# Performance work log

Hardware: AMD Instinct MI355X
Metric: run time of the kernel (lower is better)

## Reference

```python
import jax, jax.numpy as jnp
import numpy as np

B, N, C = 4, 2048, 128
H = 4
HD = C // H
SCALE = HD ** -0.5
NEG = -9e15


def setup_inputs() -> dict:
    key = jax.random.key(0)
    ks = jax.random.split(key, 6)
    x = jax.random.normal(ks[0], (B, N, C), dtype=jnp.float32)
    A = jax.random.randint(ks[1], (N, N), 0, 2, dtype=jnp.int32)
    std = 0.02
    Wq = jax.random.normal(ks[2], (C, C), dtype=jnp.float32) * std
    Wkv = jax.random.normal(ks[3], (2 * C, C), dtype=jnp.float32) * std
    Wp = jax.random.normal(ks[4], (C, C), dtype=jnp.float32) * std
    bp = jnp.zeros((C,), dtype=jnp.float32)
    return {"x": x, "A": A, "Wq": Wq, "Wkv": Wkv, "Wp": Wp, "bp": bp}


def reference(x, A, Wq, Wkv, Wp, bp):
    # q/k/v projections (torch Linear: x @ W.T)
    q = (x @ Wq.T).reshape(B, N, H, HD).transpose(0, 2, 1, 3)      # [B,H,N,HD]
    kv = (x @ Wkv.T).reshape(B, N, 2, H, HD).transpose(2, 0, 3, 1, 4)
    k, v = kv[0], kv[1]                                            # [B,H,N,HD]
    attn = jnp.einsum('bhnd,bhmd->bhnm', q, k) * SCALE             # [B,H,N,N]
    attn = jnp.where(A > 0, attn, NEG)                             # adjacency mask
    attn = jax.nn.softmax(attn, axis=-1)
    out = jnp.einsum('bhnm,bhmd->bhnd', attn, v)                   # [B,H,N,HD]
    out = out.transpose(0, 2, 1, 3).reshape(B, N, C)
    out = out @ Wp.T + bp
    return out + x                                                 # residual
```

## Files before the change

### kernel.cpp

```cpp
#include <hip/hip_runtime.h>
#include <math.h>

constexpr int kB = 4, kN = 2048, kC = 128, kH = 4, kHD = 32;
constexpr float kScaleLog2e = 0.17677669529663687f * 1.4426950408889634f;

typedef __attribute__((ext_vector_type(8))) short bf16x8;
typedef __attribute__((ext_vector_type(4))) float f32x4;

__device__ __forceinline__ float exp2fast(float x) { return __builtin_amdgcn_exp2f(x); }
__device__ __forceinline__ unsigned int cvtpk(float lo, float hi) {
  unsigned int r;
  asm("v_cvt_pk_bf16_f32 %0, %1, %2" : "=v"(r) : "v"(lo), "v"(hi));
  return r;
}
__device__ __forceinline__ float bflo(unsigned int u) {
  union { unsigned int u; float f; } v; v.u = u << 16; return v.f;
}
__device__ __forceinline__ float bfhi(unsigned int u) {
  union { unsigned int u; float f; } v; v.u = u & 0xFFFF0000u; return v.f;
}

__global__ __launch_bounds__(256) void qkv_abit_kernel(
    const float* __restrict__ x, const float* __restrict__ Wq,
    const float* __restrict__ Wkv, const int* __restrict__ A,
    unsigned short* __restrict__ qws, unsigned short* __restrict__ kws,
    unsigned short* __restrict__ vtws, unsigned long long* __restrict__ Abits) {
  const int bid = blockIdx.x;
  const int t = threadIdx.x;
  if (bid >= 512) {
    const int lane = t & 63;
    const int w0 = (bid - 512) * 4 + (t >> 6);
    for (int idx = w0; idx < kN * 32; idx += 2048) {
      const int row = idx >> 5, c0 = (idx & 31) * 64;
      unsigned long long msk = __ballot(A[(size_t)row * kN + c0 + lane] > 0);
      if (lane == 0) Abits[idx] = msk;
    }
    return;
  }
  __shared__ unsigned short xs[16][136];
  const int row0 = bid * 16;
  const int b = row0 >> 11;
  {
    const int r = t >> 4, c = (t & 15) * 8;
    const float* src = x + (size_t)(row0 + r) * kC + c;
    float4 a = *(const float4*)src;
    float4 bb = *(const float4*)(src + 4);
    *(uint4*)&xs[r][c] = make_uint4(cvtpk(a.x, a.y), cvtpk(a.z, a.w),
                                    cvtpk(bb.x, bb.y), cvtpk(bb.z, bb.w));
  }
  __syncthreads();
  const int w = t >> 6, l = t & 63, lr = l & 15, g = l >> 4;
  bf16x8 xf[4];
  #pragma unroll
  for (int s = 0; s < 4; ++s) xf[s] = *(const bf16x8*)&xs[lr][s * 32 + g * 8];
  #pragma unroll
  for (int ci = 0; ci < 6; ++ci) {
    const int c0 = (w * 6 + ci) * 16;
    const float* wrow = (c0 < 128) ? (Wq + (size_t)(c0 + lr) * kC)
                                   : (Wkv + (size_t)(c0 - 128 + lr) * kC);
    f32x4 acc = {0.f, 0.f, 0.f, 0.f};
    if (c0 < 256) {
      #pragma unroll
      for (int s = 0; s < 4; ++s) {
        const float* wp = wrow + s * 32 + g * 8;
        float4 wa = *(const float4*)wp, wb = *(const float4*)(wp + 4);
        union { uint4 u; bf16x8 v; } cw;
        cw.u = make_uint4(cvtpk(wa.x, wa.y), cvtpk(wa.z, wa.w),
                          cvtpk(wb.x, wb.y), cvtpk(wb.z, wb.w));
        acc = __builtin_amdgcn_mfma_f32_16x16x32_bf16(cw.v, xf[s], acc, 0, 0, 0);
      }
      if (c0 < 128) {
        #pragma unroll
        for (int i = 0; i < 4; ++i) acc[i] *= kScaleLog2e;
      }
      const int col0 = c0 + g * 4;
      const int h = (col0 & 127) >> 5, hd0 = col0 & 31;
      unsigned short* dst = (col0 < 128) ? qws : kws;
      uint2 pk = make_uint2(cvtpk(acc[0], acc[1]), cvtpk(acc[2], acc[3]));
      *(uint2*)&dst[((size_t)(b * kH + h) * kN + row0 + lr) * kHD + hd0] = pk;
    } else {
      #pragma unroll
      for (int s = 0; s < 4; ++s) {
        const float* wp = wrow + s * 32 + g * 8;
        float4 wa = *(const float4*)wp, wb = *(const float4*)(wp + 4);
        union { uint4 u; bf16x8 v; } cw;
        cw.u = make_uint4(cvtpk(wa.x, wa.y), cvtpk(wa.z, wa.w),
                          cvtpk(wb.x, wb.y), cvtpk(wb.z, wb.w));
        acc = __builtin_amdgcn_mfma_f32_16x16x32_bf16(xf[s], cw.v, acc, 0, 0, 0);
      }
      const int d = (c0 - 256) + lr;
      uint2 pk = make_uint2(cvtpk(acc[0], acc[1]), cvtpk(acc[2], acc[3]));
      *(uint2*)&vtws[((size_t)(b * kH + (d >> 5)) * kHD + (d & 31)) * kN + row0 + g * 4] = pk;
    }
  }
}

__global__ __launch_bounds__(256) void attn_kernel(
    const unsigned short* __restrict__ qws, const unsigned short* __restrict__ kws,
    const unsigned short* __restrict__ vtws,
    const unsigned long long* __restrict__ Abits,
    unsigned short* __restrict__ Opart, float* __restrict__ lws, int tiles) {
  __shared__ unsigned short Ksf[2][4][64][8];
  __shared__ unsigned short Vtf[2][2][2][64][8];
  __shared__ unsigned short Psf[4][2][64][8];
  const int t = threadIdx.x, w = t >> 6, l = t & 63, lr = l & 15, g = l >> 4;
  const int bh = blockIdx.y, q0 = blockIdx.x * 64, z = blockIdx.z;
  const int q = q0 + w * 16 + lr;
  const int kt0 = z * tiles;
  const unsigned short* kbase = kws + (size_t)bh * kN * kHD;
  const unsigned short* vbase = vtws + (size_t)bh * kHD * kN;
  bf16x8 qf = *(const bf16x8*)&qws[((size_t)bh * kN + q) * kHD + g * 8];
  const unsigned long long* arow = Abits + (size_t)q * (kN / 64);

  const int skc = t >> 6, sl = t & 63;
  const size_t koff = ((size_t)(skc * 16 + (sl & 15))) * kHD + (sl >> 4) * 8;
  const int sdh = t >> 7, sct = (t >> 6) & 1;
  const size_t voff = ((size_t)(sdh * 16 + (sl & 15))) * kN + sct * 32 + (sl >> 4) * 8;

  bf16x8 kreg = *(const bf16x8*)(kbase + (size_t)kt0 * 64 * kHD + koff);
  bf16x8 vreg = *(const bf16x8*)(vbase + (size_t)kt0 * 64 + voff);
  *(bf16x8*)&Ksf[0][skc][sl][0] = kreg;
  *(bf16x8*)&Vtf[0][sdh][sct][sl][0] = vreg;
  unsigned long long mw = arow[kt0], mwn = 0;

  f32x4 o0 = {0.f, 0.f, 0.f, 0.f}, o1 = {0.f, 0.f, 0.f, 0.f}, o2 = {0.f, 0.f, 0.f, 0.f};
  bf16x8 ones;
  #pragma unroll
  for (int i = 0; i < 8; ++i) ones[i] = (short)0x3F80;
  const int gsh = g * 4;
  unsigned short* const psw = &Psf[w][0][0][0];
  const int pbase = (((g >> 1) << 4) | lr) * 8 + (g & 1) * 4;

  for (int it = 0; it < tiles; ++it) {
    const int c = it & 1;
    const int kt = kt0 + it;
    __syncthreads();
    if (it + 1 < tiles) {
      kreg = *(const bf16x8*)(kbase + (size_t)(kt + 1) * 64 * kHD + koff);
      vreg = *(const bf16x8*)(vbase + (size_t)(kt + 1) * 64 + voff);
      mwn = arow[kt + 1];
    }
    const unsigned int wlo = ((unsigned int)mw) >> gsh;
    const unsigned int whi = ((unsigned int)(mw >> 32)) >> gsh;

    #pragma unroll
    for (int kc = 0; kc < 4; ++kc) {
      bf16x8 kf = *(const bf16x8*)&Ksf[c][kc][l][0];
      f32x4 acc = {0.f, 0.f, 0.f, 0.f};
      acc = __builtin_amdgcn_mfma_f32_16x16x32_bf16(kf, qf, acc, 0, 0, 0);
      const unsigned int word = (kc < 2) ? wlo : whi;
      float p[4];
      #pragma unroll
      for (int i = 0; i < 4; ++i) {
        float e = exp2fast(acc[i]);
        int msk;
        asm("v_bfe_i32 %0, %1, %2, 1" : "=v"(msk) : "v"(word), "n"((kc & 1) * 16 + i));
        union { float f; int u; } pu; pu.f = e;
        pu.u &= msk;
        p[i] = pu.f;
      }
      uint2 pk = make_uint2(cvtpk(p[0], p[1]), cvtpk(p[2], p[3]));
      *(uint2*)(psw + kc * 256 + pbase) = pk;
    }
    #pragma unroll
    for (int ct = 0; ct < 2; ++ct) {
      bf16x8 pf = *(const bf16x8*)&Psf[w][ct][l][0];
      bf16x8 va = *(const bf16x8*)&Vtf[c][0][ct][l][0];
      bf16x8 vb = *(const bf16x8*)&Vtf[c][1][ct][l][0];
      o0 = __builtin_amdgcn_mfma_f32_16x16x32_bf16(va, pf, o0, 0, 0, 0);
      o1 = __builtin_amdgcn_mfma_f32_16x16x32_bf16(vb, pf, o1, 0, 0, 0);
      o2 = __builtin_amdgcn_mfma_f32_16x16x32_bf16(ones, pf, o2, 0, 0, 0);
    }
    if (it + 1 < tiles) {
      *(bf16x8*)&Ksf[c ^ 1][skc][sl][0] = kreg;
      *(bf16x8*)&Vtf[c ^ 1][sdh][sct][sl][0] = vreg;
      mw = mwn;
    }
  }

  unsigned short* orow = Opart + ((size_t)(z * 16 + bh) * kN + q) * kHD;
  uint2 wa = make_uint2(cvtpk(o0[0], o0[1]), cvtpk(o0[2], o0[3]));
  uint2 wb = make_uint2(cvtpk(o1[0], o1[1]), cvtpk(o1[2], o1[3]));
  *(uint2*)&orow[g * 4] = wa;
  *(uint2*)&orow[16 + g * 4] = wb;
  if (g == 0) lws[(size_t)(z * 16 + bh) * kN + q] = o2[0];
}

__global__ __launch_bounds__(256) void proj_kernel(
    const unsigned short* __restrict__ Opart, const float* __restrict__ lws,
    const float* __restrict__ Wp, const float* __restrict__ bp,
    const float* __restrict__ x, float* __restrict__ out, int np) {
  const int t = threadIdx.x, w = t >> 6, l = t & 63, lr = l & 15, g = l >> 4;
  const int row0 = blockIdx.x * 16;
  const int b = row0 >> 11;
  bf16x8 af[4];
  #pragma unroll
  for (int s = 0; s < 4; ++s) {
    const int bh = b * kH + s;
    float a0 = 0.f, a1 = 0.f, a2 = 0.f, a3 = 0.f, a4 = 0.f, a5 = 0.f, a6 = 0.f, a7 = 0.f;
    float lacc = 0.f;
    for (int p = 0; p < np; ++p) {
      const size_t base = (size_t)(p * 16 + bh) * kN + row0 + lr;
      const uint4 u = *(const uint4*)&Opart[base * kHD + g * 8];
      lacc += lws[base];
      a0 += bflo(u.x); a1 += bfhi(u.x);
      a2 += bflo(u.y); a3 += bfhi(u.y);
      a4 += bflo(u.z); a5 += bfhi(u.z);
      a6 += bflo(u.w); a7 += bfhi(u.w);
    }
    const float inv = 1.f / fmaxf(lacc, 1e-30f);
    union { uint4 u; bf16x8 v; } cv;
    cv.u = make_uint4(cvtpk(a0 * inv, a1 * inv), cvtpk(a2 * inv, a3 * inv),
                      cvtpk(a4 * inv, a5 * inv), cvtpk(a6 * inv, a7 * inv));
    af[s] = cv.v;
  }
  #pragma unroll
  for (int ci = 0; ci < 2; ++ci) {
    const int c0 = (w * 2 + ci) * 16;
    const float* wrow = Wp + (size_t)(c0 + lr) * kC;
    f32x4 acc = {0.f, 0.f, 0.f, 0.f};
    #pragma unroll
    for (int s = 0; s < 4; ++s) {
      const float* wp = wrow + s * 32 + g * 8;
      float4 wa = *(const float4*)wp, wb = *(const float4*)(wp + 4);
      union { uint4 u; bf16x8 v; } cw;
      cw.u = make_uint4(cvtpk(wa.x, wa.y), cvtpk(wa.z, wa.w),
                        cvtpk(wb.x, wb.y), cvtpk(wb.z, wb.w));
      acc = __builtin_amdgcn_mfma_f32_16x16x32_bf16(cw.v, af[s], acc, 0, 0, 0);
    }
    const int col0 = c0 + g * 4;
    const size_t off = (size_t)(row0 + lr) * kC + col0;
    const float4 xb = *(const float4*)&x[off];
    const float4 bb = *(const float4*)&bp[col0];
    float4 r;
    r.x = acc[0] + bb.x + xb.x;
    r.y = acc[1] + bb.y + xb.y;
    r.z = acc[2] + bb.z + xb.z;
    r.w = acc[3] + bb.w + xb.w;
    *(float4*)&out[off] = r;
  }
}

extern "C" void kernel_launch(void* const* d_in, const int* in_sizes, int n_in,
                              void* d_out, int out_size, void* d_ws, size_t ws_size,
                              hipStream_t stream) {
  const float* x   = (const float*)d_in[0];
  const int*   A   = (const int*)d_in[1];
  const float* Wq  = (const float*)d_in[2];
  const float* Wkv = (const float*)d_in[3];
  const float* Wp  = (const float*)d_in[4];
  const float* bp  = (const float*)d_in[5];
  float* out = (float*)d_out;
  char* ws = (char*)d_ws;

  unsigned short* qws   = (unsigned short*)(ws);
  unsigned short* kws   = (unsigned short*)(ws + (2u << 20));
  unsigned short* vtws  = (unsigned short*)(ws + (4u << 20));
  unsigned long long* Abits = (unsigned long long*)(ws + (6u << 20));
  float*          lws   = (float*)(ws + (7u << 20));
  unsigned short* Opart = (unsigned short*)(ws + (8u << 20));

  const int np = (ws_size >= (16u << 20)) ? 4 : 1;
  const int tiles = 32 / np;

  qkv_abit_kernel<<<dim3(1024), dim3(256), 0, stream>>>(
      x, Wq, Wkv, A, qws, kws, vtws, Abits);
  attn_kernel<<<dim3(32, 16, np), dim3(256), 0, stream>>>(
      qws, kws, vtws, Abits, Opart, lws, tiles);
  proj_kernel<<<dim3(512), dim3(256), 0, stream>>>(Opart, lws, Wp, bp, x, out, np);
}
```

Before: 66.27 us.

## Process two query sub-tiles per wave to double K/V reuse in attention

Each wave in the attention kernel now handles 32 query rows (two 16-row MFMA tiles) instead of 16, sharing the K and V tiles loaded into LDS. The block covers 128 queries and the grid's x-dimension is halved. This amortizes K/V global loads, LDS staging and barriers over twice the work. In exchange it raises register and LDS use per block and halves the number of blocks, which may reduce occupancy or latency hiding.

```diff
diff --git a/kernel.cpp b/kernel.cpp
--- a/kernel.cpp
+++ b/kernel.cpp
@@ -102,15 +102,17 @@
     unsigned short* __restrict__ Opart, float* __restrict__ lws, int tiles) {
   __shared__ unsigned short Ksf[2][4][64][8];
   __shared__ unsigned short Vtf[2][2][2][64][8];
-  __shared__ unsigned short Psf[4][2][64][8];
+  __shared__ unsigned short Psf[4][2][2][64][8];
   const int t = threadIdx.x, w = t >> 6, l = t & 63, lr = l & 15, g = l >> 4;
-  const int bh = blockIdx.y, q0 = blockIdx.x * 64, z = blockIdx.z;
-  const int q = q0 + w * 16 + lr;
+  const int bh = blockIdx.y, q0 = blockIdx.x * 128, z = blockIdx.z;
+  const int qa = q0 + w * 32 + lr, qb = qa + 16;
   const int kt0 = z * tiles;
   const unsigned short* kbase = kws + (size_t)bh * kN * kHD;
   const unsigned short* vbase = vtws + (size_t)bh * kHD * kN;
-  bf16x8 qf = *(const bf16x8*)&qws[((size_t)bh * kN + q) * kHD + g * 8];
-  const unsigned long long* arow = Abits + (size_t)q * (kN / 64);
+  bf16x8 qf0 = *(const bf16x8*)&qws[((size_t)bh * kN + qa) * kHD + g * 8];
+  bf16x8 qf1 = *(const bf16x8*)&qws[((size_t)bh * kN + qb) * kHD + g * 8];
+  const unsigned long long* arow0 = Abits + (size_t)qa * (kN / 64);
+  const unsigned long long* arow1 = Abits + (size_t)qb * (kN / 64);
 
   const int skc = t >> 6, sl = t & 63;
   const size_t koff = ((size_t)(skc * 16 + (sl & 15))) * kHD + (sl >> 4) * 8;
@@ -121,14 +123,16 @@
   bf16x8 vreg = *(const bf16x8*)(vbase + (size_t)kt0 * 64 + voff);
   *(bf16x8*)&Ksf[0][skc][sl][0] = kreg;
   *(bf16x8*)&Vtf[0][sdh][sct][sl][0] = vreg;
-  unsigned long long mw = arow[kt0], mwn = 0;
-
-  f32x4 o0 = {0.f, 0.f, 0.f, 0.f}, o1 = {0.f, 0.f, 0.f, 0.f}, o2 = {0.f, 0.f, 0.f, 0.f};
+  unsigned long long mw0 = arow0[kt0], mw1 = arow1[kt0], mw0n = 0, mw1n = 0;
+
+  f32x4 o0a = {0.f, 0.f, 0.f, 0.f}, o1a = o0a, o2a = o0a;
+  f32x4 o0b = o0a, o1b = o0a, o2b = o0a;
   bf16x8 ones;
   #pragma unroll
   for (int i = 0; i < 8; ++i) ones[i] = (short)0x3F80;
   const int gsh = g * 4;
-  unsigned short* const psw = &Psf[w][0][0][0];
+  unsigned short* const psw0 = &Psf[w][0][0][0][0];
+  unsigned short* const psw1 = &Psf[w][1][0][0][0];
   const int pbase = (((g >> 1) << 4) | lr) * 8 + (g & 1) * 4;
 
   for (int it = 0; it < tiles; ++it) {
@@ -138,52 +142,70 @@
     if (it + 1 < tiles) {
       kreg = *(const bf16x8*)(kbase + (size_t)(kt + 1) * 64 * kHD + koff);
       vreg = *(const bf16x8*)(vbase + (size_t)(kt + 1) * 64 + voff);
-      mwn = arow[kt + 1];
-    }
-    const unsigned int wlo = ((unsigned int)mw) >> gsh;
-    const unsigned int whi = ((unsigned int)(mw >> 32)) >> gsh;
+      mw0n = arow0[kt + 1];
+      mw1n = arow1[kt + 1];
+    }
+    const unsigned int wlo0 = ((unsigned int)mw0) >> gsh;
+    const unsigned int whi0 = ((unsigned int)(mw0 >> 32)) >> gsh;
+    const unsigned int wlo1 = ((unsigned int)mw1) >> gsh;
+    const unsigned int whi1 = ((unsigned int)(mw1 >> 32)) >> gsh;
 
     #pragma unroll
     for (int kc = 0; kc < 4; ++kc) {
       bf16x8 kf = *(const bf16x8*)&Ksf[c][kc][l][0];
-      f32x4 acc = {0.f, 0.f, 0.f, 0.f};
-      acc = __builtin_amdgcn_mfma_f32_16x16x32_bf16(kf, qf, acc, 0, 0, 0);
-      const unsigned int word = (kc < 2) ? wlo : whi;
-      float p[4];
+      f32x4 z4 = {0.f, 0.f, 0.f, 0.f};
+      f32x4 acc0 = __builtin_amdgcn_mfma_f32_16x16x32_bf16(kf, qf0, z4, 0, 0, 0);
+      f32x4 acc1 = __builtin_amdgcn_mfma_f32_16x16x32_bf16(kf, qf1, z4, 0, 0, 0);
+      const unsigned int word0 = (kc < 2) ? wlo0 : whi0;
+      const unsigned int word1 = (kc < 2) ? wlo1 : whi1;
+      float p0[4], p1[4];
       #pragma unroll
       for (int i = 0; i < 4; ++i) {
-        float e = exp2fast(acc[i]);
-        int msk;
-        asm("v_bfe_i32 %0, %1, %2, 1" : "=v"(msk) : "v"(word), "n"((kc & 1) * 16 + i));
-        union { float f; int u; } pu; pu.f = e;
-        pu.u &= msk;
-        p[i] = pu.f;
-      }
-      uint2 pk = make_uint2(cvtpk(p[0], p[1]), cvtpk(p[2], p[3]));
-      *(uint2*)(psw + kc * 256 + pbase) = pk;
+        float e0 = exp2fast(acc0[i]);
+        float e1 = exp2fast(acc1[i]);
+        int m0, m1;
+        asm("v_bfe_i32 %0, %1, %2, 1" : "=v"(m0) : "v"(word0), "n"((kc & 1) * 16 + i));
+        asm("v_bfe_i32 %0, %1, %2, 1" : "=v"(m1) : "v"(word1), "n"((kc & 1) * 16 + i));
+        union { float f; int u; } u0, u1;
+        u0.f = e0; u0.u &= m0; p0[i] = u0.f;
+        u1.f = e1; u1.u &= m1; p1[i] = u1.f;
+      }
+      *(uint2*)(psw0 + kc * 256 + pbase) =
+          make_uint2(cvtpk(p0[0], p0[1]), cvtpk(p0[2], p0[3]));
+      *(uint2*)(psw1 + kc * 256 + pbase) =
+          make_uint2(cvtpk(p1[0], p1[1]), cvtpk(p1[2], p1[3]));
     }
     #pragma unroll
     for (int ct = 0; ct < 2; ++ct) {
-      bf16x8 pf = *(const bf16x8*)&Psf[w][ct][l][0];
+      bf16x8 pf0 = *(const bf16x8*)&Psf[w][0][ct][l][0];
+      bf16x8 pf1 = *(const bf16x8*)&Psf[w][1][ct][l][0];
       bf16x8 va = *(const bf16x8*)&Vtf[c][0][ct][l][0];
       bf16x8 vb = *(const bf16x8*)&Vtf[c][1][ct][l][0];
-      o0 = __builtin_amdgcn_mfma_f32_16x16x32_bf16(va, pf, o0, 0, 0, 0);
-      o1 = __builtin_amdgcn_mfma_f32_16x16x32_bf16(vb, pf, o1, 0, 0, 0);
-      o2 = __builtin_amdgcn_mfma_f32_16x16x32_bf16(ones, pf, o2, 0, 0, 0);
+      o0a = __builtin_amdgcn_mfma_f32_16x16x32_bf16(va, pf0, o0a, 0, 0, 0);
+      o1a = __builtin_amdgcn_mfma_f32_16x16x32_bf16(vb, pf0, o1a, 0, 0, 0);
+      o2a = __builtin_amdgcn_mfma_f32_16x16x32_bf16(ones, pf0, o2a, 0, 0, 0);
+      o0b = __builtin_amdgcn_mfma_f32_16x16x32_bf16(va, pf1, o0b, 0, 0, 0);
+      o1b = __builtin_amdgcn_mfma_f32_16x16x32_bf16(vb, pf1, o1b, 0, 0, 0);
+      o2b = __builtin_amdgcn_mfma_f32_16x16x32_bf16(ones, pf1, o2b, 0, 0, 0);
     }
     if (it + 1 < tiles) {
       *(bf16x8*)&Ksf[c ^ 1][skc][sl][0] = kreg;
       *(bf16x8*)&Vtf[c ^ 1][sdh][sct][sl][0] = vreg;
-      mw = mwn;
-    }
-  }
-
-  unsigned short* orow = Opart + ((size_t)(z * 16 + bh) * kN + q) * kHD;
-  uint2 wa = make_uint2(cvtpk(o0[0], o0[1]), cvtpk(o0[2], o0[3]));
-  uint2 wb = make_uint2(cvtpk(o1[0], o1[1]), cvtpk(o1[2], o1[3]));
-  *(uint2*)&orow[g * 4] = wa;
-  *(uint2*)&orow[16 + g * 4] = wb;
-  if (g == 0) lws[(size_t)(z * 16 + bh) * kN + q] = o2[0];
+      mw0 = mw0n;
+      mw1 = mw1n;
+    }
+  }
+
+  unsigned short* orow0 = Opart + ((size_t)(z * 16 + bh) * kN + qa) * kHD;
+  unsigned short* orow1 = Opart + ((size_t)(z * 16 + bh) * kN + qb) * kHD;
+  *(uint2*)&orow0[g * 4]      = make_uint2(cvtpk(o0a[0], o0a[1]), cvtpk(o0a[2], o0a[3]));
+  *(uint2*)&orow0[16 + g * 4] = make_uint2(cvtpk(o1a[0], o1a[1]), cvtpk(o1a[2], o1a[3]));
+  *(uint2*)&orow1[g * 4]      = make_uint2(cvtpk(o0b[0], o0b[1]), cvtpk(o0b[2], o0b[3]));
+  *(uint2*)&orow1[16 + g * 4] = make_uint2(cvtpk(o1b[0], o1b[1]), cvtpk(o1b[2], o1b[3]));
+  if (g == 0) {
+    lws[(size_t)(z * 16 + bh) * kN + qa] = o2a[0];
+    lws[(size_t)(z * 16 + bh) * kN + qb] = o2b[0];
+  }
 }
 
 __global__ __launch_bounds__(256) void proj_kernel(
@@ -265,7 +287,7 @@
 
   qkv_abit_kernel<<<dim3(1024), dim3(256), 0, stream>>>(
       x, Wq, Wkv, A, qws, kws, vtws, Abits);
-  attn_kernel<<<dim3(32, 16, np), dim3(256), 0, stream>>>(
+  attn_kernel<<<dim3(16, 16, np), dim3(256), 0, stream>>>(
       qws, kws, vtws, Abits, Opart, lws, tiles);
   proj_kernel<<<dim3(512), dim3(256), 0, stream>>>(Opart, lws, Wp, bp, x, out, np);
 }
```

Result: faster. 63.06 us (median of 2 runs) (-4.8%).
